# Kernel optimization log

Measured on AMD Instinct MI355X. Metric: run time of the kernel, lower is better.

The kernel has to match this reference:

```python
import jax, jax.numpy as jnp
import numpy as np

TEMP = 0.07
BASE_TEMP = 0.07
EPS = 1e-12


def setup_inputs() -> dict:
    key = jax.random.key(0)
    k1, k2, k3 = jax.random.split(key, 3)
    B, V, D, C = 4096, 1, 128, 100
    features = jax.random.normal(k1, (B, V, D), dtype=jnp.float32)
    labels = jax.random.randint(k2, (B,), 0, C, dtype=jnp.int64)
    covariances = jax.random.normal(k3, (C, D, D), dtype=jnp.float32)
    return {"features": features, "labels": labels, "covariances": covariances}


def reference(features, labels, covariances):
    B, n_views = features.shape[0], features.shape[1]
    feats = features.reshape(B, n_views, -1)
    # cat(unbind(dim=1), dim=0); with n_views==1 this is feats[:, 0]
    contrast_feature = jnp.concatenate([feats[:, v] for v in range(n_views)], axis=0)
    anchor_feature = contrast_feature  # contrast_mode == 'all'

    # mask_{i,j} = 1 if labels match
    mask = (labels[:, None] == labels[None, :]).astype(jnp.float32)  # [B,B]

    similarity_matrix = anchor_feature @ contrast_feature.T  # [B,B]

    # dis[i,j] = a_i^T C_{label_i} a_j  (gather cov per anchor, one bilinear form per pair)
    cov_g = covariances[labels]                              # [B,D,D] irregular gather
    v = jnp.einsum('id,ide->ie', anchor_feature, cov_g)      # [B,D]
    dis_matrix = v @ anchor_feature.T                        # [B,B]

    logits = (similarity_matrix + dis_matrix / (2.0 * TEMP ** 2)) / TEMP
    logits = logits - jax.lax.stop_gradient(jnp.max(logits, axis=1, keepdims=True))
    log_prob = logits - jnp.log(jnp.sum(jnp.exp(logits), axis=1, keepdims=True) + EPS)

    # original: (mask[:,:,None] * log_prob).sum(1) == mask @ log_prob (avoids B^3 temp)
    mask_sum = mask.sum(axis=1, keepdims=True)               # [B,1]
    mean_log_prob_pos = (mask @ log_prob) / (mask_sum + EPS)  # [B,B]
    loss = -(TEMP / BASE_TEMP) * mean_log_prob_pos
    return loss.mean()
```

## Files before the change

kernel.cpp:

```cpp
#include <hip/hip_runtime.h>
#include <hip/hip_bf16.h>


#define DIM 128
#define TEMP 0.07f
#define PITCH 136
#define RT 32

typedef __attribute__((ext_vector_type(8))) short short8;
typedef __attribute__((ext_vector_type(4))) float floatx4;

static __device__ __forceinline__ unsigned short f2bf(float f) {
    __hip_bfloat16 h = __float2bfloat16(f);
    union { __hip_bfloat16 h; unsigned short u; } c;
    c.h = h;
    return c.u;
}

__global__ __launch_bounds__(1024) void sort_kernel(
    const int* __restrict__ labels, int* __restrict__ order,
    int* __restrict__ classStart, int* __restrict__ counts,
    double* __restrict__ G, int B, int C) {
    __shared__ int hist[128];
    __shared__ int offs[132];
    int t = threadIdx.x;
    if (t < 128) hist[t] = 0;
    __syncthreads();
    for (int i = t; i < B; i += 1024) atomicAdd(&hist[labels[i]], 1);
    __syncthreads();
    if (t == 0) {
        int s = 0;
        for (int c = 0; c < C; ++c) { offs[c] = s; s += hist[c]; }
        offs[C] = s;
    }
    __syncthreads();
    if (t < C) {
        counts[t] = hist[t];
        G[t] = 0.0;
        classStart[t] = offs[t];
    }
    if (t == C) classStart[C] = offs[C];
    __syncthreads();
    if (t < C) hist[t] = offs[t];
    __syncthreads();
    for (int i = t; i < B; i += 1024) {
        int pos = atomicAdd(&hist[labels[i]], 1);
        order[pos] = i;
    }
}

__global__ __launch_bounds__(256) void wbuild_kernel(
    const float* __restrict__ A, const float* __restrict__ Cov,
    const int* __restrict__ order, const int* __restrict__ classStart,
    unsigned short* __restrict__ Wbf, unsigned short* __restrict__ Abf) {
    const float inv2t2 = 1.0f / (2.0f * TEMP * TEMP);
    const float invt = 1.0f / TEMP;
    const int c = blockIdx.x;
    const int start = classStart[c], end = classStart[c + 1];
    const int t = threadIdx.x;
    __shared__ float aT[DIM][RT];
    const float* CovC = Cov + (size_t)c * DIM * DIM;

    for (int r0 = start; r0 < end; r0 += RT) {
        int nr = end - r0;
        if (nr > RT) nr = RT;
        __syncthreads();
        {
            int rl = t & 31, dseg = (t >> 5) * 16;
            if (rl < nr) {
                int row = order[r0 + rl];
                const float4* src = (const float4*)(A + (size_t)row * DIM + dseg);
                float4 v[4];
#pragma unroll
                for (int i = 0; i < 4; ++i) v[i] = src[i];
                ushort4* ad = (ushort4*)(Abf + (size_t)row * DIM + dseg);
#pragma unroll
                for (int i = 0; i < 4; ++i) {
                    ushort4 o;
                    o.x = f2bf(v[i].x); o.y = f2bf(v[i].y);
                    o.z = f2bf(v[i].z); o.w = f2bf(v[i].w);
                    ad[i] = o;
                }
#pragma unroll
                for (int i = 0; i < 4; ++i) {
                    aT[dseg + i * 4 + 0][rl] = v[i].x;
                    aT[dseg + i * 4 + 1][rl] = v[i].y;
                    aT[dseg + i * 4 + 2][rl] = v[i].z;
                    aT[dseg + i * 4 + 3][rl] = v[i].w;
                }
            }
        }
        __syncthreads();
        const int rg = t >> 5, e0 = (t & 31) * 4;
        float4 acc[4];
#pragma unroll
        for (int i = 0; i < 4; ++i) acc[i] = make_float4(0.f, 0.f, 0.f, 0.f);
        const float* cp = CovC + e0;
#pragma unroll 8
        for (int d = 0; d < DIM; ++d) {
            float4 cv = *(const float4*)(cp + (size_t)d * DIM);
            float4 av = *(const float4*)&aT[d][rg * 4];
            acc[0].x = fmaf(cv.x, av.x, acc[0].x);
            acc[0].y = fmaf(cv.y, av.x, acc[0].y);
            acc[0].z = fmaf(cv.z, av.x, acc[0].z);
            acc[0].w = fmaf(cv.w, av.x, acc[0].w);
            acc[1].x = fmaf(cv.x, av.y, acc[1].x);
            acc[1].y = fmaf(cv.y, av.y, acc[1].y);
            acc[1].z = fmaf(cv.z, av.y, acc[1].z);
            acc[1].w = fmaf(cv.w, av.y, acc[1].w);
            acc[2].x = fmaf(cv.x, av.z, acc[2].x);
            acc[2].y = fmaf(cv.y, av.z, acc[2].y);
            acc[2].z = fmaf(cv.z, av.z, acc[2].z);
            acc[2].w = fmaf(cv.w, av.z, acc[2].w);
            acc[3].x = fmaf(cv.x, av.w, acc[3].x);
            acc[3].y = fmaf(cv.y, av.w, acc[3].y);
            acc[3].z = fmaf(cv.z, av.w, acc[3].z);
            acc[3].w = fmaf(cv.w, av.w, acc[3].w);
        }
#pragma unroll
        for (int rr = 0; rr < 4; ++rr) {
            int rl2 = rg * 4 + rr;
            if (rl2 < nr) {
                int row = order[r0 + rl2];
                float ax = aT[e0 + 0][rl2], ay = aT[e0 + 1][rl2];
                float az = aT[e0 + 2][rl2], aw = aT[e0 + 3][rl2];
                ushort4 w;
                w.x = f2bf((ax + acc[rr].x * inv2t2) * invt);
                w.y = f2bf((ay + acc[rr].y * inv2t2) * invt);
                w.z = f2bf((az + acc[rr].z * inv2t2) * invt);
                w.w = f2bf((aw + acc[rr].w * inv2t2) * invt);
                *(ushort4*)(Wbf + (size_t)row * DIM + e0) = w;
            }
        }
    }
}

__global__ __launch_bounds__(256, 2) void main_kernel(
    const unsigned short* __restrict__ Wbf, const unsigned short* __restrict__ Abf,
    float* __restrict__ mP, float* __restrict__ zP, float* __restrict__ sP,
    int Jsplit, int JSWEEP, int nP) {
    __shared__ __align__(16) unsigned short sW[128 * PITCH];
    __shared__ __align__(16) unsigned short sA[64 * PITCH];

    const int mb = blockIdx.x / Jsplit;
    const int jsp = blockIdx.x % Jsplit;
    const int rowBase = mb * 128;
    const int t = threadIdx.x;
    const int wave = t >> 6, lane = t & 63, quad = lane >> 4, l16 = lane & 15;
    const int waveM = wave >> 1, waveN = wave & 1;

    {
        int row = t >> 1, half = t & 1;
        const unsigned short* src = Wbf + (size_t)(rowBase + row) * DIM + half * 64;
        unsigned short* dst = sW + row * PITCH + half * 64;
#pragma unroll
        for (int i = 0; i < 8; i++)
            *(short8*)(dst + i * 8) = *(const short8*)(src + i * 8);
    }

    float run_m[4][4], run_Z[4][4], run_s[4][4];
#pragma unroll
    for (int a = 0; a < 4; a++)
#pragma unroll
        for (int r = 0; r < 4; r++) {
            run_m[a][r] = -3.4e38f; run_Z[a][r] = 0.f; run_s[a][r] = 0.f;
        }

    const unsigned short* myW = sW + (waveM * 64 + l16) * PITCH;
    const unsigned short* myA = sA + (waveN * 32 + l16) * PITCH;

    for (int js = 0; js < JSWEEP; ++js) {
        __syncthreads();
        {
            int row = t >> 2, q = t & 3;
            int j0 = (jsp * JSWEEP + js) * 64;
            const unsigned short* src = Abf + (size_t)(j0 + row) * DIM + q * 32;
            unsigned short* dst = sA + row * PITCH + q * 32;
#pragma unroll
            for (int i = 0; i < 4; i++)
                *(short8*)(dst + i * 8) = *(const short8*)(src + i * 8);
        }
        __syncthreads();

        floatx4 acc[4][2];
#pragma unroll
        for (int mt = 0; mt < 4; mt++)
#pragma unroll
            for (int nt = 0; nt < 2; nt++) acc[mt][nt] = (floatx4)0.f;

#pragma unroll
        for (int kst = 0; kst < 4; ++kst) {
            const int koff = kst * 32 + quad * 8;
            short8 bfrag[2];
#pragma unroll
            for (int nt = 0; nt < 2; nt++)
                bfrag[nt] = *(const short8*)(myA + nt * 16 * PITCH + koff);
#pragma unroll
            for (int mt = 0; mt < 4; mt++) {
                short8 afrag = *(const short8*)(myW + mt * 16 * PITCH + koff);
#pragma unroll
                for (int nt = 0; nt < 2; nt++)
                    acc[mt][nt] = __builtin_amdgcn_mfma_f32_16x16x32_bf16(
                        afrag, bfrag[nt], acc[mt][nt], 0, 0, 0);
            }
        }

#pragma unroll
        for (int mt = 0; mt < 4; mt++)
#pragma unroll
            for (int r = 0; r < 4; r++) {
                float v0 = acc[mt][0][r], v1 = acc[mt][1][r];
                float tm = fmaxf(v0, v1);
                float nm = fmaxf(run_m[mt][r], tm);
                run_Z[mt][r] = run_Z[mt][r] * __expf(run_m[mt][r] - nm)
                             + __expf(v0 - nm) + __expf(v1 - nm);
                run_m[mt][r] = nm;
                run_s[mt][r] += v0 + v1;
            }
    }

    const int chunk = jsp * 2 + waveN;
#pragma unroll
    for (int mt = 0; mt < 4; mt++)
#pragma unroll
        for (int r = 0; r < 4; r++) {
            float m = run_m[mt][r], Z = run_Z[mt][r], s = run_s[mt][r];
#pragma unroll
            for (int mask = 1; mask < 16; mask <<= 1) {
                float om = __shfl_xor(m, mask);
                float oZ = __shfl_xor(Z, mask);
                float os = __shfl_xor(s, mask);
                float nm = fmaxf(m, om);
                Z = Z * __expf(m - nm) + oZ * __expf(om - nm);
                m = nm;
                s += os;
            }
            if (l16 == r) {
                int row = rowBase + waveM * 64 + mt * 16 + quad * 4 + r;
                size_t idx = (size_t)row * nP + chunk;
                mP[idx] = m; zP[idx] = Z; sP[idx] = s;
            }
        }
}

__global__ __launch_bounds__(64) void combine_kernel(
    const float* __restrict__ mP, const float* __restrict__ zP,
    const float* __restrict__ sP, const int* __restrict__ labels,
    double* __restrict__ G, int B, int nP) {
    int k = blockIdx.x;
    int l = threadIdx.x;
    float m = -3.4e38f, Z = 0.0f, s = 0.0f;
    if (l < nP) {
        size_t idx = (size_t)k * nP + l;
        m = mP[idx]; Z = zP[idx]; s = sP[idx];
    }
    float M = m;
#pragma unroll
    for (int o = 32; o > 0; o >>= 1) M = fmaxf(M, __shfl_xor(M, o));
    float zt = Z * __expf(m - M);
    float st = s;
#pragma unroll
    for (int o = 32; o > 0; o >>= 1) {
        zt += __shfl_xor(zt, o);
        st += __shfl_xor(st, o);
    }
    if (l == 0) {
        double Sk = (double)st - (double)B * (double)M
                    - (double)B * log((double)zt + 1e-12);
        atomicAdd(&G[labels[k]], Sk);
    }
}

__global__ __launch_bounds__(128) void final_kernel(
    const double* __restrict__ G, const int* __restrict__ counts,
    float* __restrict__ out, int C, double invB2) {
    __shared__ double sh[128];
    int t = threadIdx.x;
    double v = 0.0;
    if (t < C) {
        double cnt = (double)counts[t];
        v = G[t] * (cnt / (cnt + 1e-12));
    }
    sh[t] = v;
    __syncthreads();
    for (int o = 64; o > 0; o >>= 1) {
        if (t < o) sh[t] += sh[t + o];
        __syncthreads();
    }
    if (t == 0) out[0] = (float)(-sh[0] * invB2);
}

extern "C" void kernel_launch(void* const* d_in, const int* in_sizes, int n_in,
                              void* d_out, int out_size, void* d_ws, size_t ws_size,
                              hipStream_t stream) {
    const float* A = (const float*)d_in[0];
    const int* labels = (const int*)d_in[1];
    const float* Cov = (const float*)d_in[2];
    float* out = (float*)d_out;

    int B = in_sizes[0] / DIM;
    int C = in_sizes[2] / (DIM * DIM);
    int Jsplit = 16;
    int JSWEEP = B / (Jsplit * 64);
    int nP = Jsplit * 2;

    char* ws = (char*)d_ws;
    unsigned short* Wbf = (unsigned short*)ws;
    unsigned short* Abf = Wbf + (size_t)B * DIM;
    float* mP = (float*)(Abf + (size_t)B * DIM);
    float* zP = mP + (size_t)B * nP;
    float* sP = zP + (size_t)B * nP;
    double* G = (double*)(sP + (size_t)B * nP);
    int* counts = (int*)(G + C);
    int* order = counts + C;
    int* classStart = order + B;

    sort_kernel<<<1, 1024, 0, stream>>>(labels, order, classStart, counts,
                                        G, B, C);
    wbuild_kernel<<<C, 256, 0, stream>>>(A, Cov, order, classStart, Wbf, Abf);
    main_kernel<<<(B / 128) * Jsplit, 256, 0, stream>>>(Wbf, Abf, mP, zP, sP,
                                                        Jsplit, JSWEEP, nP);
    combine_kernel<<<B, 64, 0, stream>>>(mP, zP, sP, labels, G, B, nP);
    final_kernel<<<1, 128, 0, stream>>>(G, counts, out, C,
                                        1.0 / ((double)B * (double)B));
}
```

Before: 113.1 us.

## Parallelize W build per class tile, fuse final reduction, scan offsets

Four changes land together. The W-build kernel now launches TILES blocks per class, each handling one 32-row tile, instead of one block looping over all rows of its class. The final reduction kernel is folded into the combine kernel through a last-block ticket counter, which removes one launch. The serial class-offset loop in the sort kernel becomes a wave-level shuffle scan, and the main kernel gets a smaller LDS pitch and a higher occupancy hint. The tiling silently assumes no class has more than TILES*RT rows, and the pitch change may alter LDS bank-conflict behaviour.

```diff
diff --git a/kernel.cpp b/kernel.cpp
--- a/kernel.cpp
+++ b/kernel.cpp
@@ -4,8 +4,9 @@
 
 #define DIM 128
 #define TEMP 0.07f
-#define PITCH 136
+#define PITCH 132
 #define RT 32
+#define TILES 4
 
 typedef __attribute__((ext_vector_type(8))) short short8;
 typedef __attribute__((ext_vector_type(4))) float floatx4;
@@ -20,28 +21,38 @@
 __global__ __launch_bounds__(1024) void sort_kernel(
     const int* __restrict__ labels, int* __restrict__ order,
     int* __restrict__ classStart, int* __restrict__ counts,
-    double* __restrict__ G, int B, int C) {
+    double* __restrict__ G, int* __restrict__ ticket, int B, int C) {
     __shared__ int hist[128];
-    __shared__ int offs[132];
+    __shared__ int offs[128];
+    __shared__ int w0tot;
     int t = threadIdx.x;
     if (t < 128) hist[t] = 0;
     __syncthreads();
     for (int i = t; i < B; i += 1024) atomicAdd(&hist[labels[i]], 1);
     __syncthreads();
-    if (t == 0) {
-        int s = 0;
-        for (int c = 0; c < C; ++c) { offs[c] = s; s += hist[c]; }
-        offs[C] = s;
-    }
-    __syncthreads();
-    if (t < C) {
-        counts[t] = hist[t];
-        G[t] = 0.0;
-        classStart[t] = offs[t];
-    }
-    if (t == C) classStart[C] = offs[C];
-    __syncthreads();
-    if (t < C) hist[t] = offs[t];
+    if (t < 128) {
+        int h = hist[t];
+        int v = h;
+        int lane = t & 63;
+#pragma unroll
+        for (int o = 1; o < 64; o <<= 1) {
+            int u = __shfl_up(v, o);
+            if (lane >= o) v += u;
+        }
+        if (t == 63) w0tot = v;
+        __syncthreads();
+        if (t >= 64) v += w0tot;
+        offs[t] = v - h;
+    } else {
+        __syncthreads();
+    }
+    __syncthreads();
+    if (t < 128) {
+        if (t <= C) classStart[t] = (t < 128) ? offs[t] : 0;
+        if (t < C) { counts[t] = hist[t]; G[t] = 0.0; }
+        if (t == 127) *ticket = 0;
+        hist[t] = offs[t];
+    }
     __syncthreads();
     for (int i = t; i < B; i += 1024) {
         int pos = atomicAdd(&hist[labels[i]], 1);
@@ -55,87 +66,87 @@
     unsigned short* __restrict__ Wbf, unsigned short* __restrict__ Abf) {
     const float inv2t2 = 1.0f / (2.0f * TEMP * TEMP);
     const float invt = 1.0f / TEMP;
-    const int c = blockIdx.x;
-    const int start = classStart[c], end = classStart[c + 1];
+    const int c = blockIdx.x / TILES;
+    const int tile = blockIdx.x % TILES;
+    const int r0 = classStart[c] + tile * RT;
+    const int end = classStart[c + 1];
+    if (r0 >= end) return;
+    int nr = end - r0;
+    if (nr > RT) nr = RT;
     const int t = threadIdx.x;
     __shared__ float aT[DIM][RT];
     const float* CovC = Cov + (size_t)c * DIM * DIM;
 
-    for (int r0 = start; r0 < end; r0 += RT) {
-        int nr = end - r0;
-        if (nr > RT) nr = RT;
-        __syncthreads();
-        {
-            int rl = t & 31, dseg = (t >> 5) * 16;
-            if (rl < nr) {
-                int row = order[r0 + rl];
-                const float4* src = (const float4*)(A + (size_t)row * DIM + dseg);
-                float4 v[4];
-#pragma unroll
-                for (int i = 0; i < 4; ++i) v[i] = src[i];
-                ushort4* ad = (ushort4*)(Abf + (size_t)row * DIM + dseg);
-#pragma unroll
-                for (int i = 0; i < 4; ++i) {
-                    ushort4 o;
-                    o.x = f2bf(v[i].x); o.y = f2bf(v[i].y);
-                    o.z = f2bf(v[i].z); o.w = f2bf(v[i].w);
-                    ad[i] = o;
-                }
-#pragma unroll
-                for (int i = 0; i < 4; ++i) {
-                    aT[dseg + i * 4 + 0][rl] = v[i].x;
-                    aT[dseg + i * 4 + 1][rl] = v[i].y;
-                    aT[dseg + i * 4 + 2][rl] = v[i].z;
-                    aT[dseg + i * 4 + 3][rl] = v[i].w;
-                }
-            }
-        }
-        __syncthreads();
-        const int rg = t >> 5, e0 = (t & 31) * 4;
-        float4 acc[4];
-#pragma unroll
-        for (int i = 0; i < 4; ++i) acc[i] = make_float4(0.f, 0.f, 0.f, 0.f);
-        const float* cp = CovC + e0;
+    {
+        int rl = t & 31, dseg = (t >> 5) * 16;
+        if (rl < nr) {
+            int row = order[r0 + rl];
+            const float4* src = (const float4*)(A + (size_t)row * DIM + dseg);
+            float4 v[4];
+#pragma unroll
+            for (int i = 0; i < 4; ++i) v[i] = src[i];
+            ushort4* ad = (ushort4*)(Abf + (size_t)row * DIM + dseg);
+#pragma unroll
+            for (int i = 0; i < 4; ++i) {
+                ushort4 o;
+                o.x = f2bf(v[i].x); o.y = f2bf(v[i].y);
+                o.z = f2bf(v[i].z); o.w = f2bf(v[i].w);
+                ad[i] = o;
+            }
+#pragma unroll
+            for (int i = 0; i < 4; ++i) {
+                aT[dseg + i * 4 + 0][rl] = v[i].x;
+                aT[dseg + i * 4 + 1][rl] = v[i].y;
+                aT[dseg + i * 4 + 2][rl] = v[i].z;
+                aT[dseg + i * 4 + 3][rl] = v[i].w;
+            }
+        }
+    }
+    __syncthreads();
+    const int rg = t >> 5, e0 = (t & 31) * 4;
+    float4 acc[4];
+#pragma unroll
+    for (int i = 0; i < 4; ++i) acc[i] = make_float4(0.f, 0.f, 0.f, 0.f);
+    const float* cp = CovC + e0;
 #pragma unroll 8
-        for (int d = 0; d < DIM; ++d) {
-            float4 cv = *(const float4*)(cp + (size_t)d * DIM);
-            float4 av = *(const float4*)&aT[d][rg * 4];
-            acc[0].x = fmaf(cv.x, av.x, acc[0].x);
-            acc[0].y = fmaf(cv.y, av.x, acc[0].y);
-            acc[0].z = fmaf(cv.z, av.x, acc[0].z);
-            acc[0].w = fmaf(cv.w, av.x, acc[0].w);
-            acc[1].x = fmaf(cv.x, av.y, acc[1].x);
-            acc[1].y = fmaf(cv.y, av.y, acc[1].y);
-            acc[1].z = fmaf(cv.z, av.y, acc[1].z);
-            acc[1].w = fmaf(cv.w, av.y, acc[1].w);
-            acc[2].x = fmaf(cv.x, av.z, acc[2].x);
-            acc[2].y = fmaf(cv.y, av.z, acc[2].y);
-            acc[2].z = fmaf(cv.z, av.z, acc[2].z);
-            acc[2].w = fmaf(cv.w, av.z, acc[2].w);
-            acc[3].x = fmaf(cv.x, av.w, acc[3].x);
-            acc[3].y = fmaf(cv.y, av.w, acc[3].y);
-            acc[3].z = fmaf(cv.z, av.w, acc[3].z);
-            acc[3].w = fmaf(cv.w, av.w, acc[3].w);
-        }
-#pragma unroll
-        for (int rr = 0; rr < 4; ++rr) {
-            int rl2 = rg * 4 + rr;
-            if (rl2 < nr) {
-                int row = order[r0 + rl2];
-                float ax = aT[e0 + 0][rl2], ay = aT[e0 + 1][rl2];
-                float az = aT[e0 + 2][rl2], aw = aT[e0 + 3][rl2];
-                ushort4 w;
-                w.x = f2bf((ax + acc[rr].x * inv2t2) * invt);
-                w.y = f2bf((ay + acc[rr].y * inv2t2) * invt);
-                w.z = f2bf((az + acc[rr].z * inv2t2) * invt);
-                w.w = f2bf((aw + acc[rr].w * inv2t2) * invt);
-                *(ushort4*)(Wbf + (size_t)row * DIM + e0) = w;
-            }
-        }
-    }
-}
-
-__global__ __launch_bounds__(256, 2) void main_kernel(
+    for (int d = 0; d < DIM; ++d) {
+        float4 cv = *(const float4*)(cp + (size_t)d * DIM);
+        float4 av = *(const float4*)&aT[d][rg * 4];
+        acc[0].x = fmaf(cv.x, av.x, acc[0].x);
+        acc[0].y = fmaf(cv.y, av.x, acc[0].y);
+        acc[0].z = fmaf(cv.z, av.x, acc[0].z);
+        acc[0].w = fmaf(cv.w, av.x, acc[0].w);
+        acc[1].x = fmaf(cv.x, av.y, acc[1].x);
+        acc[1].y = fmaf(cv.y, av.y, acc[1].y);
+        acc[1].z = fmaf(cv.z, av.y, acc[1].z);
+        acc[1].w = fmaf(cv.w, av.y, acc[1].w);
+        acc[2].x = fmaf(cv.x, av.z, acc[2].x);
+        acc[2].y = fmaf(cv.y, av.z, acc[2].y);
+        acc[2].z = fmaf(cv.z, av.z, acc[2].z);
+        acc[2].w = fmaf(cv.w, av.z, acc[2].w);
+        acc[3].x = fmaf(cv.x, av.w, acc[3].x);
+        acc[3].y = fmaf(cv.y, av.w, acc[3].y);
+        acc[3].z = fmaf(cv.z, av.w, acc[3].z);
+        acc[3].w = fmaf(cv.w, av.w, acc[3].w);
+    }
+#pragma unroll
+    for (int rr = 0; rr < 4; ++rr) {
+        int rl2 = rg * 4 + rr;
+        if (rl2 < nr) {
+            int row = order[r0 + rl2];
+            float ax = aT[e0 + 0][rl2], ay = aT[e0 + 1][rl2];
+            float az = aT[e0 + 2][rl2], aw = aT[e0 + 3][rl2];
+            ushort4 w;
+            w.x = f2bf((ax + acc[rr].x * inv2t2) * invt);
+            w.y = f2bf((ay + acc[rr].y * inv2t2) * invt);
+            w.z = f2bf((az + acc[rr].z * inv2t2) * invt);
+            w.w = f2bf((aw + acc[rr].w * inv2t2) * invt);
+            *(ushort4*)(Wbf + (size_t)row * DIM + e0) = w;
+        }
+    }
+}
+
+__global__ __launch_bounds__(256, 3) void main_kernel(
     const unsigned short* __restrict__ Wbf, const unsigned short* __restrict__ Abf,
     float* __restrict__ mP, float* __restrict__ zP, float* __restrict__ sP,
     int Jsplit, int JSWEEP, int nP) {
@@ -243,51 +254,59 @@
         }
 }
 
-__global__ __launch_bounds__(64) void combine_kernel(
+__global__ __launch_bounds__(128) void combine_kernel(
     const float* __restrict__ mP, const float* __restrict__ zP,
     const float* __restrict__ sP, const int* __restrict__ labels,
-    double* __restrict__ G, int B, int nP) {
+    double* __restrict__ G, const int* __restrict__ counts,
+    int* __restrict__ ticket, float* __restrict__ out,
+    int B, int nP, int C) {
+    __shared__ int flag;
+    __shared__ double sh[128];
     int k = blockIdx.x;
-    int l = threadIdx.x;
-    float m = -3.4e38f, Z = 0.0f, s = 0.0f;
-    if (l < nP) {
-        size_t idx = (size_t)k * nP + l;
-        m = mP[idx]; Z = zP[idx]; s = sP[idx];
-    }
-    float M = m;
-#pragma unroll
-    for (int o = 32; o > 0; o >>= 1) M = fmaxf(M, __shfl_xor(M, o));
-    float zt = Z * __expf(m - M);
-    float st = s;
-#pragma unroll
-    for (int o = 32; o > 0; o >>= 1) {
-        zt += __shfl_xor(zt, o);
-        st += __shfl_xor(st, o);
-    }
-    if (l == 0) {
-        double Sk = (double)st - (double)B * (double)M
-                    - (double)B * log((double)zt + 1e-12);
-        atomicAdd(&G[labels[k]], Sk);
-    }
-}
-
-__global__ __launch_bounds__(128) void final_kernel(
-    const double* __restrict__ G, const int* __restrict__ counts,
-    float* __restrict__ out, int C, double invB2) {
-    __shared__ double sh[128];
     int t = threadIdx.x;
-    double v = 0.0;
-    if (t < C) {
-        double cnt = (double)counts[t];
-        v = G[t] * (cnt / (cnt + 1e-12));
-    }
-    sh[t] = v;
-    __syncthreads();
-    for (int o = 64; o > 0; o >>= 1) {
-        if (t < o) sh[t] += sh[t + o];
-        __syncthreads();
-    }
-    if (t == 0) out[0] = (float)(-sh[0] * invB2);
+    if (t < 64) {
+        float m = -3.4e38f, Z = 0.0f, s = 0.0f;
+        if (t < nP) {
+            size_t idx = (size_t)k * nP + t;
+            m = mP[idx]; Z = zP[idx]; s = sP[idx];
+        }
+        float M = m;
+#pragma unroll
+        for (int o = 32; o > 0; o >>= 1) M = fmaxf(M, __shfl_xor(M, o));
+        float zt = Z * __expf(m - M);
+        float st = s;
+#pragma unroll
+        for (int o = 32; o > 0; o >>= 1) {
+            zt += __shfl_xor(zt, o);
+            st += __shfl_xor(st, o);
+        }
+        if (t == 0) {
+            double Sk = (double)st - (double)B * (double)M
+                        - (double)B * log((double)zt + 1e-12);
+            atomicAdd(&G[labels[k]], Sk);
+        }
+    }
+    __threadfence();
+    __syncthreads();
+    if (t == 0) flag = (atomicAdd(ticket, 1) == (int)gridDim.x - 1);
+    __syncthreads();
+    if (flag) {
+        __threadfence();
+        double v = 0.0;
+        if (t < C) {
+            double g = atomicAdd(&G[t], 0.0);
+            double cnt = (double)counts[t];
+            v = g * (cnt / (cnt + 1e-12));
+        }
+        sh[t] = v;
+        __syncthreads();
+        for (int o = 64; o > 0; o >>= 1) {
+            if (t < o) sh[t] += sh[t + o];
+            __syncthreads();
+        }
+        if (t == 0)
+            out[0] = (float)(-sh[0] / ((double)B * (double)B));
+    }
 }
 
 extern "C" void kernel_launch(void* const* d_in, const int* in_sizes, int n_in,
@@ -314,13 +333,14 @@
     int* counts = (int*)(G + C);
     int* order = counts + C;
     int* classStart = order + B;
+    int* ticket = classStart + C + 1;
 
     sort_kernel<<<1, 1024, 0, stream>>>(labels, order, classStart, counts,
-                                        G, B, C);
-    wbuild_kernel<<<C, 256, 0, stream>>>(A, Cov, order, classStart, Wbf, Abf);
+                                        G, ticket, B, C);
+    wbuild_kernel<<<C * TILES, 256, 0, stream>>>(A, Cov, order, classStart,
+                                                 Wbf, Abf);
     main_kernel<<<(B / 128) * Jsplit, 256, 0, stream>>>(Wbf, Abf, mP, zP, sP,
                                                         Jsplit, JSWEEP, nP);
-    combine_kernel<<<B, 64, 0, stream>>>(mP, zP, sP, labels, G, B, nP);
-    final_kernel<<<1, 128, 0, stream>>>(G, counts, out, C,
-                                        1.0 / ((double)B * (double)B));
-}
+    combine_kernel<<<B, 128, 0, stream>>>(mP, zP, sP, labels, G, counts,
+                                          ticket, out, B, nP, C);
+}
```

After: 262.6 us. +132.3%, slower.
